# Kernel tuning notes

Hardware: AMD Instinct MI355X
Metric: run time of the kernel (lower is better)

Reference implementation:

```python
import jax, jax.numpy as jnp
import numpy as np

KERNEL_MUL = 2.0
KERNEL_NUM = 5
EPS = 1e-6
MU, SIGMA = 18.0, 8.0


def setup_inputs() -> dict:
    key = jax.random.key(0)
    k1, k2 = jax.random.split(key)
    N = 4096
    source = jax.random.uniform(k1, (N, 3), dtype=jnp.float32)
    target = jax.random.uniform(k2, (N, 3), dtype=jnp.float32)
    return {"source": source, "target": target}


def _confidence_weights(x):
    # x: [N, 3] columns (v, alpha, beta)
    v, alpha, beta = x[:, 0], x[:, 1], x[:, 2]
    phi = 2.0 * v + alpha + 1.0 / (beta + EPS)
    w = jnp.exp(-((phi - MU) ** 2) / (2.0 * SIGMA ** 2))
    w = w / (w.sum() + EPS)
    return jax.lax.stop_gradient(w)  # .detach() in torch


def reference(source, target):
    sw = _confidence_weights(source)
    tw = _confidence_weights(target)

    ns = source.shape[0]
    total = jnp.concatenate([source, target], axis=0)  # [2N, 3]
    n_total = total.shape[0]

    # pairwise squared L2 via the gram trick (same math as expand-subtract)
    sq = jnp.sum(total * total, axis=1)                      # [2N]
    L2 = sq[:, None] + sq[None, :] - 2.0 * (total @ total.T)  # [2N, 2N]

    # bandwidth from detached distances (torch uses L2_distance.data)
    bandwidth = jax.lax.stop_gradient(jnp.sum(L2)) / (n_total ** 2 - n_total)
    bandwidth = bandwidth / (KERNEL_MUL ** (KERNEL_NUM // 2))

    # the loss only touches the XY/YX cross blocks; YX = XY^T so their sums
    # are equal -> compute the kernel on the cross block only.
    L2_xy = L2[:ns, ns:]  # [ns, nt]
    kernel_xy = jnp.zeros_like(L2_xy)
    for i in range(KERNEL_NUM):
        kernel_xy = kernel_xy + jnp.exp(-L2_xy / (bandwidth * KERNEL_MUL ** i))

    weight_xy = sw[:, None] * tw[None, :]
    loss = -2.0 * jnp.sum(kernel_xy * weight_xy)  # -sum(XY) - sum(YX)
    return loss
```

## Files before the change

### kernel.cpp

```cpp
#include <hip/hip_runtime.h>
#include <math.h>

#define EPSF 1e-6f

__device__ __forceinline__ float fexp2(float x) {
    return __builtin_amdgcn_exp2f(x);
}

__device__ __forceinline__ float conf_w(float x, float y, float z) {
    float phi = 2.f * x + y + 1.f / (z + EPSF);
    float dphi = phi - 18.f;
    return expf(-(dphi * dphi) * (1.f / 128.f));
}

__global__ __launch_bounds__(1024) void mainK(
    const float* __restrict__ src, const float* __restrict__ tgt, int n,
    double* __restrict__ mainP, double* __restrict__ swtw)
{
    const int tid = threadIdx.x;
    const int bid = blockIdx.x;

    __shared__ double red[16][6];
    __shared__ double fsum[6];
    __shared__ float4 tg[256];
    __shared__ double wsum[16];

    double a0 = 0, a1 = 0, a2 = 0, a3 = 0, a4 = 0, a5 = 0;
    for (int i = tid; i < 2 * n; i += 1024) {
        const float* p = (i < n) ? (src + 3 * i) : (tgt + 3 * (i - n));
        float x = p[0], y = p[1], z = p[2];
        float w = conf_w(x, y, z);
        a0 += (double)(x * x + y * y + z * z);
        a1 += (double)x; a2 += (double)y; a3 += (double)z;
        if (i < n) a4 += (double)w; else a5 += (double)w;
    }
    double acc[6] = {a0, a1, a2, a3, a4, a5};
    #pragma unroll
    for (int k = 0; k < 6; ++k) {
        double v = acc[k];
        for (int off = 32; off > 0; off >>= 1) v += __shfl_down(v, off);
        if ((tid & 63) == 0) red[tid >> 6][k] = v;
    }
    __syncthreads();
    if (tid < 6) {
        double s = 0.0;
        #pragma unroll
        for (int wv = 0; wv < 16; ++wv) s += red[wv][tid];
        fsum[tid] = s;
    }
    __syncthreads();
    double S0 = fsum[0], Sx = fsum[1], Sy = fsum[2], Sz = fsum[3];

    double ntf = 2.0 * (double)n;
    double sumL2 = 2.0 * ntf * S0 - 2.0 * (Sx * Sx + Sy * Sy + Sz * Sz);
    double bw = sumL2 / (ntf * ntf - ntf) * 0.25;
    float m = (float)(-1.4426950408889634 / bw);

    if (bid == 0 && tid == 0) { swtw[0] = fsum[4]; swtw[1] = fsum[5]; }

    int bx = bid >> 4, by = bid & 15;
    if (tid < 256) {
        const float* p = tgt + 3 * ((by << 8) + tid);
        float x = p[0], y = p[1], z = p[2];
        tg[tid] = make_float4(x, y, z, conf_w(x, y, z));
    }
    __syncthreads();

    int s = tid & 255;
    int c = tid >> 8;
    const float* p = src + 3 * ((bx << 8) + s);
    float sx = p[0], sy = p[1], sz = p[2];
    float sw = conf_w(sx, sy, sz);
    float acc0 = 0.f;
    int j0 = c << 6;
    #pragma unroll 8
    for (int jj = 0; jj < 64; ++jj) {
        float4 t = tg[j0 + jj];
        float dx = sx - t.x, dy = sy - t.y, dz = sz - t.z;
        float d = dx * dx + dy * dy + dz * dz;
        float u = d * m;
        float e4 = fexp2(u * 0.0625f);
        float e3 = e4 * e4;
        float e2 = e3 * e3;
        float e1 = e2 * e2;
        float e0 = e1 * e1;
        acc0 += t.w * (e0 + e1 + e2 + e3 + e4);
    }
    double v = (double)(acc0 * sw);
    for (int off = 32; off > 0; off >>= 1) v += __shfl_down(v, off);
    if ((tid & 63) == 0) wsum[tid >> 6] = v;
    __syncthreads();
    if (tid == 0) {
        double tot = 0.0;
        #pragma unroll
        for (int wv = 0; wv < 16; ++wv) tot += wsum[wv];
        mainP[bid] = tot;
    }
}

__global__ __launch_bounds__(256) void finK(
    const double* __restrict__ mainP, const double* __restrict__ swtw,
    float* __restrict__ out)
{
    const int tid = threadIdx.x;
    __shared__ double wsum[4];
    double a = mainP[tid];
    for (int off = 32; off > 0; off >>= 1) a += __shfl_down(a, off);
    if ((tid & 63) == 0) wsum[tid >> 6] = a;
    __syncthreads();
    if (tid == 0) {
        double tot = wsum[0] + wsum[1] + wsum[2] + wsum[3];
        double denom = (swtw[0] + (double)EPSF) * (swtw[1] + (double)EPSF);
        out[0] = (float)(-2.0 * tot / denom);
    }
}

extern "C" void kernel_launch(void* const* d_in, const int* in_sizes, int n_in,
                              void* d_out, int out_size, void* d_ws, size_t ws_size,
                              hipStream_t stream) {
    const float* src = (const float*)d_in[0];
    const float* tgt = (const float*)d_in[1];
    int n = in_sizes[0] / 3;
    float* out = (float*)d_out;

    double* mainP = (double*)d_ws;
    double* swtw = mainP + 256;

    mainK<<<256, 1024, 0, stream>>>(src, tgt, n, mainP, swtw);
    finK<<<1, 256, 0, stream>>>(mainP, swtw, out);
}
```

Baseline: 72.46 us.

## Fuse final reduction via atomic counter, double grid, use gram-form distance

Drops the separate finalize kernel: each block atomically adds its partial sum, and the last block to arrive, detected with an atomic counter, writes the loss. The grid grows to 512 blocks, each covering 128 targets, so every block repeats the full statistics pass over all points. The inner loop computes the scaled squared distance as precomputed norms plus FMAs. This adds a memset launch and more redundant prologue work, and changes floating-point summation order.

```diff
diff --git a/kernel.cpp b/kernel.cpp
--- a/kernel.cpp
+++ b/kernel.cpp
@@ -15,14 +15,16 @@
 
 __global__ __launch_bounds__(1024) void mainK(
     const float* __restrict__ src, const float* __restrict__ tgt, int n,
-    double* __restrict__ mainP, double* __restrict__ swtw)
+    double* __restrict__ acc, unsigned* __restrict__ counter,
+    float* __restrict__ out)
 {
     const int tid = threadIdx.x;
     const int bid = blockIdx.x;
 
     __shared__ double red[16][6];
     __shared__ double fsum[6];
-    __shared__ float4 tg[256];
+    __shared__ float4 tg[128];
+    __shared__ float mt[128];
     __shared__ double wsum[16];
 
     double a0 = 0, a1 = 0, a2 = 0, a3 = 0, a4 = 0, a5 = 0;
@@ -34,10 +36,10 @@
         a1 += (double)x; a2 += (double)y; a3 += (double)z;
         if (i < n) a4 += (double)w; else a5 += (double)w;
     }
-    double acc[6] = {a0, a1, a2, a3, a4, a5};
+    double av[6] = {a0, a1, a2, a3, a4, a5};
     #pragma unroll
     for (int k = 0; k < 6; ++k) {
-        double v = acc[k];
+        double v = av[k];
         for (int off = 32; off > 0; off >>= 1) v += __shfl_down(v, off);
         if ((tid & 63) == 0) red[tid >> 6][k] = v;
     }
@@ -56,13 +58,12 @@
     double bw = sumL2 / (ntf * ntf - ntf) * 0.25;
     float m = (float)(-1.4426950408889634 / bw);
 
-    if (bid == 0 && tid == 0) { swtw[0] = fsum[4]; swtw[1] = fsum[5]; }
-
-    int bx = bid >> 4, by = bid & 15;
-    if (tid < 256) {
-        const float* p = tgt + 3 * ((by << 8) + tid);
+    int bx = bid >> 5, by = bid & 31;
+    if (tid < 128) {
+        const float* p = tgt + 3 * ((by << 7) + tid);
         float x = p[0], y = p[1], z = p[2];
         tg[tid] = make_float4(x, y, z, conf_w(x, y, z));
+        mt[tid] = m * (x * x + y * y + z * z);
     }
     __syncthreads();
 
@@ -71,14 +72,18 @@
     const float* p = src + 3 * ((bx << 8) + s);
     float sx = p[0], sy = p[1], sz = p[2];
     float sw = conf_w(sx, sy, sz);
+    float n2m = -2.f * m;
+    float sxm = n2m * sx, sym = n2m * sy, szm = n2m * sz;
+    float base = m * (sx * sx + sy * sy + sz * sz);
     float acc0 = 0.f;
-    int j0 = c << 6;
+    int j0 = c << 5;
     #pragma unroll 8
-    for (int jj = 0; jj < 64; ++jj) {
+    for (int jj = 0; jj < 32; ++jj) {
         float4 t = tg[j0 + jj];
-        float dx = sx - t.x, dy = sy - t.y, dz = sz - t.z;
-        float d = dx * dx + dy * dy + dz * dz;
-        float u = d * m;
+        float h = fmaf(t.x, sxm, base);
+        h = fmaf(t.y, sym, h);
+        h = fmaf(t.z, szm, h);
+        float u = h + mt[j0 + jj];
         float e4 = fexp2(u * 0.0625f);
         float e3 = e4 * e4;
         float e2 = e3 * e3;
@@ -90,28 +95,20 @@
     for (int off = 32; off > 0; off >>= 1) v += __shfl_down(v, off);
     if ((tid & 63) == 0) wsum[tid >> 6] = v;
     __syncthreads();
+
     if (tid == 0) {
         double tot = 0.0;
         #pragma unroll
         for (int wv = 0; wv < 16; ++wv) tot += wsum[wv];
-        mainP[bid] = tot;
-    }
-}
-
-__global__ __launch_bounds__(256) void finK(
-    const double* __restrict__ mainP, const double* __restrict__ swtw,
-    float* __restrict__ out)
-{
-    const int tid = threadIdx.x;
-    __shared__ double wsum[4];
-    double a = mainP[tid];
-    for (int off = 32; off > 0; off >>= 1) a += __shfl_down(a, off);
-    if ((tid & 63) == 0) wsum[tid >> 6] = a;
-    __syncthreads();
-    if (tid == 0) {
-        double tot = wsum[0] + wsum[1] + wsum[2] + wsum[3];
-        double denom = (swtw[0] + (double)EPSF) * (swtw[1] + (double)EPSF);
-        out[0] = (float)(-2.0 * tot / denom);
+        atomicAdd(acc, tot);
+        __threadfence();
+        unsigned old = atomicAdd(counter, 1u);
+        if (old == (unsigned)(gridDim.x - 1)) {
+            double total = atomicAdd(acc, 0.0);
+            double Sw = fsum[4], Tw = fsum[5];
+            out[0] = (float)(-2.0 * total /
+                             ((Sw + (double)EPSF) * (Tw + (double)EPSF)));
+        }
     }
 }
 
@@ -123,9 +120,9 @@
     int n = in_sizes[0] / 3;
     float* out = (float*)d_out;
 
-    double* mainP = (double*)d_ws;
-    double* swtw = mainP + 256;
+    double* acc = (double*)d_ws;
+    unsigned* counter = (unsigned*)((char*)d_ws + sizeof(double));
 
-    mainK<<<256, 1024, 0, stream>>>(src, tgt, n, mainP, swtw);
-    finK<<<1, 256, 0, stream>>>(mainP, swtw, out);
+    hipMemsetAsync(d_ws, 0, 16, stream);
+    mainK<<<512, 1024, 0, stream>>>(src, tgt, n, acc, counter, out);
 }
```

Measured after the change: 82.53 us. 13.9% more time.
